# Kernel optimization log

Measured on AMD Instinct MI355X. Metric: run time of the kernel, lower is better.

The kernel has to match this reference:

```python
import jax, jax.numpy as jnp
import numpy as np

B, S, E, H = 16, 2048, 512, 64


def setup_inputs() -> dict:
    key = jax.random.key(0)
    k1, k2, k3, k4, k5 = jax.random.split(key, 5)
    inp = {
        "input": jax.random.normal(k1, (B, S, E), dtype=jnp.float32),
        "seq_lengths": jax.random.randint(k2, (B,), 0, S).astype(jnp.int64),
        "Wq": jax.random.normal(k3, (E, H), dtype=jnp.float32) * (1.0 / np.sqrt(E)),
        "Wk": jax.random.normal(k4, (E, H), dtype=jnp.float32) * (1.0 / np.sqrt(E)),
        "Wv": jax.random.normal(k5, (E, H), dtype=jnp.float32) * (1.0 / np.sqrt(E)),
    }
    return inp


def reference(input, seq_lengths, Wq, Wk, Wv):
    # Projections (bias-free Linear): [B,S,E] @ [E,H] -> [B,S,H]
    q = input @ Wq
    k = input @ Wk
    v = input @ Wv
    Sdim = input.shape[1]
    head_size = Wk.shape[-1]
    # Padding mask: position >= seq_length -> True. Zero out q and k (NOT v),
    # exactly as the torch module does with masked_fill.
    pad = (jnp.arange(Sdim)[None, :] >= seq_lengths[:, None])[:, :, None]  # [B,S,1]
    q = jnp.where(pad, 0.0, q)
    k = jnp.where(pad, 0.0, k)
    scale = 1.0 / np.sqrt(head_size).astype(np.float32)
    # Full score matrix [B,S,S] (the memory-bound intermediate)
    scores = jnp.einsum("bsh,bth->bst", q, k) * scale
    weights = jax.nn.softmax(scores, axis=-1)
    weights = jnp.where(jnp.isnan(weights), 0.0, weights)
    out = jnp.einsum("bst,bth->bsh", weights, v)  # [B,S,H]
    return out
```

## Files before the change

kernel.cpp:

```cpp
#include <hip/hip_runtime.h>
#include <hip/hip_bf16.h>

typedef __bf16 bf16;
typedef __bf16 bf16x8 __attribute__((ext_vector_type(8)));
typedef __bf16 bf16x4 __attribute__((ext_vector_type(4)));
typedef float  f32x4  __attribute__((ext_vector_type(4)));
typedef float  f32x16 __attribute__((ext_vector_type(16)));
typedef unsigned int u32x4 __attribute__((ext_vector_type(4)));

static constexpr int SDIM = 2048;
static constexpr int EDIM = 512;
static constexpr int HDIM = 64;

typedef __attribute__((address_space(1))) const void* gptr_t;
typedef __attribute__((address_space(3))) void*       lptr_t;

__device__ __forceinline__ void gl_lds16(const bf16* g, bf16* l) {
  __builtin_amdgcn_global_load_lds((gptr_t)g, (lptr_t)l, 16, 0, 0);
}

#if __has_builtin(__builtin_amdgcn_exp2f)
#define EXP2F(x) __builtin_amdgcn_exp2f(x)
#else
#define EXP2F(x) exp2f(x)
#endif

__device__ __forceinline__ bf16x8 pack8(f32x4 a, f32x4 b) {
  bf16x8 r;
  r[0] = (bf16)a[0]; r[1] = (bf16)a[1]; r[2] = (bf16)a[2]; r[3] = (bf16)a[3];
  r[4] = (bf16)b[0]; r[5] = (bf16)b[1]; r[6] = (bf16)b[2]; r[7] = (bf16)b[3];
  return r;
}

__device__ __forceinline__ unsigned cvtpk_bf16(float a, float b) {
  unsigned r;
  asm("v_cvt_pk_bf16_f32 %0, %1, %2" : "=v"(r) : "v"(a), "v"(b));
  return r;
}

__global__ __launch_bounds__(256) void wt_kernel(const float* __restrict__ Wq,
                                                 const float* __restrict__ Wk,
                                                 const float* __restrict__ Wv,
                                                 bf16* __restrict__ Wt) {
  __shared__ float lds[64][65];
  const int mat = blockIdx.x >> 3;
  const int et  = blockIdx.x & 7;
  const float* W = (mat == 0) ? Wq : ((mat == 1) ? Wk : Wv);
  const float scale = (mat == 0) ? 0.18033688f : 1.0f;
  const int t  = threadIdx.x;
  const int er = t >> 2;
  const int c4 = (t & 3) * 16;
#pragma unroll
  for (int j = 0; j < 4; ++j) {
    f32x4 v = *(const f32x4*)(W + (size_t)(et * 64 + er) * HDIM + c4 + j * 4);
    lds[er][c4 + j * 4 + 0] = v[0]; lds[er][c4 + j * 4 + 1] = v[1];
    lds[er][c4 + j * 4 + 2] = v[2]; lds[er][c4 + j * 4 + 3] = v[3];
  }
  __syncthreads();
  const int h  = t >> 2;
  const int ec = (t & 3) * 16;
  bf16x8 o0, o1;
#pragma unroll
  for (int j = 0; j < 8; ++j) o0[j] = (bf16)(lds[ec + j][h] * scale);
#pragma unroll
  for (int j = 0; j < 8; ++j) o1[j] = (bf16)(lds[ec + 8 + j][h] * scale);
  bf16* dst = Wt + mat * (HDIM * EDIM) + (size_t)h * EDIM + et * 64 + ec;
  *(bf16x8*)dst = o0;
  *(bf16x8*)(dst + 8) = o1;
}

__global__ __launch_bounds__(256) void proj_kernel(const float* __restrict__ x,
                                                   const bf16* __restrict__ Wt,
                                                   const int* __restrict__ lens,
                                                   bf16* __restrict__ qo,
                                                   bf16* __restrict__ ko,
                                                   bf16* __restrict__ vT) {
  __shared__ __align__(16) bf16 wbuf[2][192 * 64];
  const int tid  = threadIdx.x;
  const int wave = tid >> 6;
  const int lane = tid & 63;
  const int quad = lane >> 4;
  const int l16  = lane & 15;
  const int rowbase = blockIdx.x * 64 + wave * 16;
  const int b = blockIdx.x >> 5;
  const float* xrow = x + (size_t)(rowbase + l16) * EDIM + quad * 8;
  const int srow   = lane >> 3;
  const int schunk = (lane & 7) ^ srow;

  #define WSTAGE(ck, buf) { _Pragma("unroll")                                  \
    for (int i6 = 0; i6 < 6; ++i6) {                                           \
      const int R0 = (wave * 6 + i6) * 8;                                      \
      gl_lds16(Wt + (size_t)(R0 + srow) * EDIM + (ck) * 64 + schunk * 8,       \
               &(buf)[R0 * 64]); } }

  f32x4 acc[3][4];
#pragma unroll
  for (int m = 0; m < 3; ++m)
#pragma unroll
    for (int nt = 0; nt < 4; ++nt) acc[m][nt] = (f32x4){0.f, 0.f, 0.f, 0.f};

  #define WCOMPUTE(buf, eo4, afrag) { _Pragma("unroll")                        \
    for (int m = 0; m < 3; ++m) { _Pragma("unroll")                            \
      for (int nt = 0; nt < 4; ++nt) {                                         \
        bf16x8 bfv = *(const bf16x8*)(&(buf)[(m * 64 + nt * 16 + l16) * 64 +   \
                                             ((((eo4) + quad) ^ (l16 & 7)) * 8)]); \
        acc[m][nt] = __builtin_amdgcn_mfma_f32_16x16x32_bf16(afrag, bfv, acc[m][nt], 0, 0, 0); } } }

  WSTAGE(0, wbuf[0]);
  __builtin_amdgcn_sched_barrier(0);
  f32x4 c0 = *(const f32x4*)(xrow);
  f32x4 c1 = *(const f32x4*)(xrow + 4);
  f32x4 c2 = *(const f32x4*)(xrow + 32);
  f32x4 c3 = *(const f32x4*)(xrow + 36);
  f32x4 n0 = *(const f32x4*)(xrow + 64);
  f32x4 n1 = *(const f32x4*)(xrow + 68);
  f32x4 n2 = *(const f32x4*)(xrow + 96);
  f32x4 n3 = *(const f32x4*)(xrow + 100);
  __builtin_amdgcn_sched_barrier(0);
  asm volatile("s_waitcnt vmcnt(8)" ::: "memory");
  __builtin_amdgcn_s_barrier();
  __builtin_amdgcn_sched_barrier(0);

#pragma unroll
  for (int ck = 0; ck < 8; ++ck) {
    const int cs = (ck < 7) ? (ck + 1) : 7;
    WSTAGE(cs, wbuf[(ck + 1) & 1]);
    __builtin_amdgcn_sched_barrier(0);
    const int kf = (ck < 6) ? (ck + 2) : 7;
    f32x4 m0 = *(const f32x4*)(xrow + kf * 64);
    f32x4 m1 = *(const f32x4*)(xrow + kf * 64 + 4);
    f32x4 m2 = *(const f32x4*)(xrow + kf * 64 + 32);
    f32x4 m3 = *(const f32x4*)(xrow + kf * 64 + 36);
    __builtin_amdgcn_sched_barrier(0);
    bf16x8 a = pack8(c0, c1);
    WCOMPUTE(wbuf[ck & 1], 0, a);
    a = pack8(c2, c3);
    WCOMPUTE(wbuf[ck & 1], 4, a);
    c0 = n0; c1 = n1; c2 = n2; c3 = n3;
    n0 = m0; n1 = m1; n2 = m2; n3 = m3;
    asm volatile("s_waitcnt vmcnt(4)" ::: "memory");
    __builtin_amdgcn_s_barrier();
    __builtin_amdgcn_sched_barrier(0);
  }

  int odd_or = 0;
#pragma unroll
  for (int i = 1; i < 16; i += 2) odd_or |= lens[i];
  const int len = (odd_or == 0) ? lens[2 * b] : lens[b];

#pragma unroll
  for (int nt = 0; nt < 4; ++nt) {
    const int h = nt * 16 + l16;
    bf16x4 vv;
#pragma unroll
    for (int r = 0; r < 4; ++r) {
      const int row = rowbase + quad * 4 + r;
      const int s = row & (SDIM - 1);
      const bool pad = (s >= len);
      qo[(size_t)row * HDIM + h] = (bf16)(pad ? 0.f : acc[0][nt][r]);
      ko[(size_t)row * HDIM + h] = (bf16)(pad ? 0.f : acc[1][nt][r]);
      vv[r] = (bf16)acc[2][nt][r];
    }
    *(bf16x4*)(vT + ((size_t)b * HDIM + h) * SDIM + (rowbase & (SDIM - 1)) + quad * 4) = vv;
  }
  #undef WSTAGE
  #undef WCOMPUTE
}

__global__ __launch_bounds__(256) void attn_kernel(const bf16* __restrict__ qb,
                                                   const bf16* __restrict__ kb,
                                                   const bf16* __restrict__ vT,
                                                   float* __restrict__ out) {
  __shared__ __align__(16) bf16 Kbuf[2][2][64 * 64];
  __shared__ __align__(16) bf16 Vbuf[2][2][64 * 64];
  const int tid  = threadIdx.x;
  const int wave = tid >> 6;
  const int lane = tid & 63;
  const int hi   = lane >> 5;
  const int l32  = lane & 31;
  const int iq   = wave & 1;
  const int jk   = wave >> 1;
  const int xcd = blockIdx.x & 7;
  const int jj  = blockIdx.x >> 3;
  const int b   = xcd * 2 + (jj >> 5);
  const int qbase = (jj & 31) * 64 + iq * 32;
  const bf16* q0 = qb + (size_t)b * SDIM * HDIM;
  const bf16* k0 = kb + (size_t)b * SDIM * HDIM;
  const bf16* v0 = vT + (size_t)b * HDIM * SDIM;
  const int srow   = lane >> 3;
  const int schunk = (lane & 7) ^ srow;
  const int rswz   = (l32 & 7) << 4;

  bf16x8 qf[4];
#pragma unroll
  for (int c = 0; c < 4; ++c)
    qf[c] = *(const bf16x8*)(q0 + (size_t)(qbase + l32) * HDIM + c * 16 + hi * 8);

  f32x16 O[2];
#pragma unroll
  for (int ht = 0; ht < 2; ++ht)
#pragma unroll
    for (int r = 0; r < 16; ++r) O[ht][r] = 0.f;
  float l_acc = 0.f;

  bf16x8 paP[4];
  bf16x8 vfP[2][4];

  #define STAGE(sidx, db) {                                                    \
    const int key0_ = (wave & 1) * 1024 + (sidx) * 64;                         \
    if (wave < 2) {                                                            \
      const bf16* gk = k0 + (size_t)(key0_ + srow) * HDIM + schunk * 8;        \
      bf16* lk = &Kbuf[db][wave & 1][0];                                       \
      _Pragma("unroll")                                                        \
      for (int r8 = 0; r8 < 8; ++r8)                                           \
        gl_lds16(gk + (size_t)r8 * 8 * HDIM, lk + r8 * 8 * 64);                \
    } else {                                                                   \
      const bf16* gv = v0 + (size_t)srow * SDIM + key0_ + schunk * 8;          \
      bf16* lv = &Vbuf[db][wave & 1][0];                                       \
      _Pragma("unroll")                                                        \
      for (int r8 = 0; r8 < 8; ++r8)                                           \
        gl_lds16(gv + (size_t)r8 * 8 * SDIM, lv + r8 * 8 * 64);                \
    }                                                                          \
  }

  STAGE(0, 0);
#pragma unroll 2
  for (int s = 0; s < 16; ++s) {
    __syncthreads();
    if (s + 1 < 16) STAGE(s + 1, (s + 1) & 1);
    const bf16* KB = &Kbuf[s & 1][jk][0];
    const bf16* VB = &Vbuf[s & 1][jk][0];

    bf16x8 kf[2][4];
#pragma unroll
    for (int kt = 0; kt < 2; ++kt)
#pragma unroll
      for (int c = 0; c < 4; ++c)
        kf[kt][c] = *(const bf16x8*)((const char*)KB + (kt * 32 + l32) * 128 +
                                     ((c * 32 + hi * 16) ^ rswz));

    if (s) {
#pragma unroll
      for (int ht = 0; ht < 2; ++ht)
#pragma unroll
        for (int tc = 0; tc < 4; ++tc)
          O[ht] = __builtin_amdgcn_mfma_f32_32x32x16_bf16(paP[tc], vfP[ht][tc], O[ht], 0, 0, 0);
    }

    bf16x8 paC[4];
#pragma unroll
    for (int kt = 0; kt < 2; ++kt) {
      f32x16 st;
#pragma unroll
      for (int r = 0; r < 16; ++r) st[r] = 0.f;
#pragma unroll
      for (int c = 0; c < 4; ++c)
        st = __builtin_amdgcn_mfma_f32_32x32x16_bf16(kf[kt][c], qf[c], st, 0, 0, 0);
      float p[16];
#pragma unroll
      for (int r = 0; r < 16; ++r) p[r] = EXP2F(st[r]);
      float s0 = (p[0] + p[1]) + (p[2] + p[3]);
      float s1 = (p[4] + p[5]) + (p[6] + p[7]);
      float s2 = (p[8] + p[9]) + (p[10] + p[11]);
      float s3 = (p[12] + p[13]) + (p[14] + p[15]);
      l_acc += (s0 + s1) + (s2 + s3);
      unsigned u0 = cvtpk_bf16(p[0], p[1]);
      unsigned u1 = cvtpk_bf16(p[2], p[3]);
      unsigned u2 = cvtpk_bf16(p[4], p[5]);
      unsigned u3 = cvtpk_bf16(p[6], p[7]);
      asm("v_permlane32_swap_b32 %0, %1" : "+v"(u0), "+v"(u2));
      asm("v_permlane32_swap_b32 %0, %1" : "+v"(u1), "+v"(u3));
      union { u32x4 u; bf16x8 v; } f0;
      f0.u[0] = u0; f0.u[1] = u1; f0.u[2] = u2; f0.u[3] = u3;
      paC[kt * 2 + 0] = f0.v;
      unsigned u4 = cvtpk_bf16(p[8],  p[9]);
      unsigned u5 = cvtpk_bf16(p[10], p[11]);
      unsigned u6 = cvtpk_bf16(p[12], p[13]);
      unsigned u7 = cvtpk_bf16(p[14], p[15]);
      asm("v_permlane32_swap_b32 %0, %1" : "+v"(u4), "+v"(u6));
      asm("v_permlane32_swap_b32 %0, %1" : "+v"(u5), "+v"(u7));
      union { u32x4 u; bf16x8 v; } f1;
      f1.u[0] = u4; f1.u[1] = u5; f1.u[2] = u6; f1.u[3] = u7;
      paC[kt * 2 + 1] = f1.v;
    }

#pragma unroll
    for (int ht = 0; ht < 2; ++ht)
#pragma unroll
      for (int tc = 0; tc < 4; ++tc)
        vfP[ht][tc] = *(const bf16x8*)((const char*)VB + (ht * 32 + l32) * 128 +
                                       ((tc * 32 + hi * 16) ^ rswz));
#pragma unroll
    for (int i = 0; i < 4; ++i) paP[i] = paC[i];
  }

#pragma unroll
  for (int ht = 0; ht < 2; ++ht)
#pragma unroll
    for (int tc = 0; tc < 4; ++tc)
      O[ht] = __builtin_amdgcn_mfma_f32_32x32x16_bf16(paP[tc], vfP[ht][tc], O[ht], 0, 0, 0);

  l_acc += __shfl_xor(l_acc, 32);

  float* cb = (float*)&Kbuf[0][0][0];
  float* cl = (float*)&Vbuf[0][0][0];
  __syncthreads();
  if (jk == 1) {
#pragma unroll
    for (int ht = 0; ht < 2; ++ht)
#pragma unroll
      for (int r = 0; r < 16; ++r) {
        const int qrow = (r & 3) + 8 * (r >> 2) + 4 * hi;
        cb[(iq * 32 + qrow) * 64 + ht * 32 + l32] = O[ht][r];
      }
    if (hi == 0) cl[iq * 32 + l32] = l_acc;
  }
  __syncthreads();
  if (jk == 0) {
    const float inv_own = 1.0f / (l_acc + cl[iq * 32 + l32]);
#pragma unroll
    for (int r = 0; r < 16; ++r) {
      const int qrow = (r & 3) + 8 * (r >> 2) + 4 * hi;
      const float inv = __shfl(inv_own, qrow);
#pragma unroll
      for (int ht = 0; ht < 2; ++ht) {
        const float val = (O[ht][r] + cb[(iq * 32 + qrow) * 64 + ht * 32 + l32]) * inv;
        out[((size_t)b * SDIM + qbase + qrow) * HDIM + ht * 32 + l32] = val;
      }
    }
  }
  #undef STAGE
}

extern "C" void kernel_launch(void* const* d_in, const int* in_sizes, int n_in,
                              void* d_out, int out_size, void* d_ws, size_t ws_size,
                              hipStream_t stream) {
  (void)in_sizes; (void)n_in; (void)out_size; (void)ws_size;
  const float* x  = (const float*)d_in[0];
  const int*   sl = (const int*)d_in[1];
  const float* Wq = (const float*)d_in[2];
  const float* Wk = (const float*)d_in[3];
  const float* Wv = (const float*)d_in[4];
  float* out = (float*)d_out;

  char* ws = (char*)d_ws;
  bf16* Wt = (bf16*)(ws);
  bf16* qb = (bf16*)(ws + (256 << 10));
  bf16* kb = (bf16*)(ws + (256 << 10) + (4 << 20));
  bf16* vT = (bf16*)(ws + (256 << 10) + (8 << 20));

  wt_kernel  <<<24,  256, 0, stream>>>(Wq, Wk, Wv, Wt);
  proj_kernel<<<512, 256, 0, stream>>>(x, Wt, sl, qb, kb, vT);
  attn_kernel<<<512, 256, 0, stream>>>(qb, kb, vT, out);
}
```

Measured before the change: 136.6 us.

## Load V fragments directly from global memory and raise MFMA wave priority

V no longer goes through LDS. Each wave now reads its V^T fragments straight from global memory into registers, and all four waves share the K staging into LDS (4 loads each instead of 8 for two waves). This halves LDS use and spreads the async copy work across waves. s_setprio brackets are also added around the MFMA groups so matrix work is favoured over the exp/pack work of other waves. The risk is that the direct global V loads add latency on the critical path inside the loop, and each wave redundantly fetches V that was previously shared via LDS.

```diff
diff --git a/kernel.cpp b/kernel.cpp
--- a/kernel.cpp
+++ b/kernel.cpp
@@ -172,7 +172,6 @@
                                                    const bf16* __restrict__ vT,
                                                    float* __restrict__ out) {
   __shared__ __align__(16) bf16 Kbuf[2][2][64 * 64];
-  __shared__ __align__(16) bf16 Vbuf[2][2][64 * 64];
   const int tid  = threadIdx.x;
   const int wave = tid >> 6;
   const int lane = tid & 63;
@@ -207,20 +206,14 @@
   bf16x8 vfP[2][4];
 
   #define STAGE(sidx, db) {                                                    \
-    const int key0_ = (wave & 1) * 1024 + (sidx) * 64;                         \
-    if (wave < 2) {                                                            \
-      const bf16* gk = k0 + (size_t)(key0_ + srow) * HDIM + schunk * 8;        \
-      bf16* lk = &Kbuf[db][wave & 1][0];                                       \
-      _Pragma("unroll")                                                        \
-      for (int r8 = 0; r8 < 8; ++r8)                                           \
-        gl_lds16(gk + (size_t)r8 * 8 * HDIM, lk + r8 * 8 * 64);                \
-    } else {                                                                   \
-      const bf16* gv = v0 + (size_t)srow * SDIM + key0_ + schunk * 8;          \
-      bf16* lv = &Vbuf[db][wave & 1][0];                                       \
-      _Pragma("unroll")                                                        \
-      for (int r8 = 0; r8 < 8; ++r8)                                           \
-        gl_lds16(gv + (size_t)r8 * 8 * SDIM, lv + r8 * 8 * 64);                \
-    }                                                                          \
+    const int half_ = wave >> 1;                                               \
+    const int key0_ = half_ * 1024 + (sidx) * 64;                              \
+    const int rb_   = (wave & 1) * 32;                                         \
+    const bf16* gk = k0 + (size_t)(key0_ + rb_ + srow) * HDIM + schunk * 8;    \
+    bf16* lk = &Kbuf[db][half_][rb_ * 64];                                     \
+    _Pragma("unroll")                                                          \
+    for (int j4 = 0; j4 < 4; ++j4)                                             \
+      gl_lds16(gk + (size_t)j4 * 8 * HDIM, lk + j4 * 8 * 64);                  \
   }
 
   STAGE(0, 0);
@@ -229,7 +222,6 @@
     __syncthreads();
     if (s + 1 < 16) STAGE(s + 1, (s + 1) & 1);
     const bf16* KB = &Kbuf[s & 1][jk][0];
-    const bf16* VB = &Vbuf[s & 1][jk][0];
 
     bf16x8 kf[2][4];
 #pragma unroll
@@ -240,11 +232,13 @@
                                      ((c * 32 + hi * 16) ^ rswz));
 
     if (s) {
+      __builtin_amdgcn_s_setprio(1);
 #pragma unroll
       for (int ht = 0; ht < 2; ++ht)
 #pragma unroll
         for (int tc = 0; tc < 4; ++tc)
           O[ht] = __builtin_amdgcn_mfma_f32_32x32x16_bf16(paP[tc], vfP[ht][tc], O[ht], 0, 0, 0);
+      __builtin_amdgcn_s_setprio(0);
     }
 
     bf16x8 paC[4];
@@ -253,9 +247,11 @@
       f32x16 st;
 #pragma unroll
       for (int r = 0; r < 16; ++r) st[r] = 0.f;
+      __builtin_amdgcn_s_setprio(1);
 #pragma unroll
       for (int c = 0; c < 4; ++c)
         st = __builtin_amdgcn_mfma_f32_32x32x16_bf16(kf[kt][c], qf[c], st, 0, 0, 0);
+      __builtin_amdgcn_s_setprio(0);
       float p[16];
 #pragma unroll
       for (int r = 0; r < 16; ++r) p[r] = EXP2F(st[r]);
@@ -284,26 +280,31 @@
       paC[kt * 2 + 1] = f1.v;
     }
 
-#pragma unroll
-    for (int ht = 0; ht < 2; ++ht)
-#pragma unroll
-      for (int tc = 0; tc < 4; ++tc)
-        vfP[ht][tc] = *(const bf16x8*)((const char*)VB + (ht * 32 + l32) * 128 +
-                                       ((tc * 32 + hi * 16) ^ rswz));
+    {
+      const bf16* vg = v0 + jk * 1024 + s * 64;
+#pragma unroll
+      for (int ht = 0; ht < 2; ++ht)
+#pragma unroll
+        for (int tc = 0; tc < 4; ++tc)
+          vfP[ht][tc] = *(const bf16x8*)(vg + (size_t)(ht * 32 + l32) * SDIM +
+                                         tc * 16 + hi * 8);
+    }
 #pragma unroll
     for (int i = 0; i < 4; ++i) paP[i] = paC[i];
   }
 
+  __builtin_amdgcn_s_setprio(1);
 #pragma unroll
   for (int ht = 0; ht < 2; ++ht)
 #pragma unroll
     for (int tc = 0; tc < 4; ++tc)
       O[ht] = __builtin_amdgcn_mfma_f32_32x32x16_bf16(paP[tc], vfP[ht][tc], O[ht], 0, 0, 0);
+  __builtin_amdgcn_s_setprio(0);
 
   l_acc += __shfl_xor(l_acc, 32);
 
   float* cb = (float*)&Kbuf[0][0][0];
-  float* cl = (float*)&Vbuf[0][0][0];
+  float* cl = (float*)&Kbuf[1][0][0];
   __syncthreads();
   if (jk == 1) {
 #pragma unroll
```

Measured after the change: 148.0 us. +8.3%, slower.
